# Kernel tuning notes

Measured on AMD Instinct MI355X. Metric: run time of the kernel, lower is better.

The kernel has to match this reference:

```python
import jax, jax.numpy as jnp
import numpy as np

B, T, C, H, D = 4, 2048, 1024, 16, 64  # batch, seq, n_embd, n_head, head_size


def setup_inputs() -> dict:
    key = jax.random.key(0)
    ks = jax.random.split(key, 8)
    s = 0.02  # init scale for weights
    return {
        "q": jax.random.normal(ks[0], (B, T, C), jnp.float32),
        "k": jax.random.normal(ks[1], (B, T, C), jnp.float32),
        "v": jax.random.normal(ks[2], (B, T, C), jnp.float32),
        "Wq": jax.random.normal(ks[3], (H, C, D), jnp.float32) * s,
        "Wk": jax.random.normal(ks[4], (H, C, D), jnp.float32) * s,
        "Wv": jax.random.normal(ks[5], (H, C, D), jnp.float32) * s,
        "Wo": jax.random.normal(ks[6], (H * D, C), jnp.float32) * s,
        "bo": jnp.zeros((C,), jnp.float32),
    }


def reference(q, k, v, Wq, Wk, Wv, Wo, bo):
    # Per-head projections (vectorized over heads): [B,T,C] x [H,C,D] -> [B,H,T,D]
    qh = jnp.einsum('btc,hcd->bhtd', q, Wq)
    kh = jnp.einsum('btc,hcd->bhtd', k, Wk)
    vh = jnp.einsum('btc,hcd->bhtd', v, Wv)
    # NOTE: source divides by sqrt(C) = sqrt(n_embd), not sqrt(head_size)
    scale = 1.0 / jnp.sqrt(jnp.float32(C))
    att = jnp.einsum('bhtd,bhsd->bhts', qh, kh) * scale  # [B,H,T,T]
    causal = jnp.tril(jnp.ones((T, T), dtype=bool))
    att = jnp.where(causal, att, -jnp.inf)
    p = jax.nn.softmax(att, axis=-1)  # dropout is identity in eval mode
    out = jnp.einsum('bhts,bhsd->bhtd', p, vh)
    # concat heads in order: [B,H,T,D] -> [B,T,H*D]
    out = out.transpose(0, 2, 1, 3).reshape(B, T, H * D)
    return out @ Wo + bo
```

## Files before the change

kernel.cpp:

```cpp
#include <hip/hip_runtime.h>
#include <hip/hip_bf16.h>
#include <cstdint>
#include <cstddef>

#define B_  4
#define T_  2048
#define C_  1024
#define H_  16
#define D_  64
#define MROWS (B_*T_)
#define NDIM  (H_*D_)

typedef float  f32x4 __attribute__((ext_vector_type(4)));
typedef __bf16 bfrag __attribute__((ext_vector_type(8)));

__device__ __forceinline__ unsigned short f2bf(float f) {
  union { float f; unsigned u; } v; v.f = f;
  unsigned r = v.u + 0x7fffu + ((v.u >> 16) & 1u);
  return (unsigned short)(r >> 16);
}

__device__ __forceinline__ void async_load16(const void* g, void* l) {
  __builtin_amdgcn_global_load_lds((__attribute__((address_space(1))) void*)(void*)g,
                                   (__attribute__((address_space(3))) void*)l,
                                   16, 0, 0);
}

__device__ __forceinline__ unsigned cvt_pk_bf16(float f0, float f1) {
  unsigned r;
  asm("v_cvt_pk_bf16_f32 %0, %1, %2" : "=v"(r) : "v"(f0), "v"(f1));
  return r;
}

__global__ __launch_bounds__(256) void prep_kernel(
    const float* __restrict__ q, const float* __restrict__ k, const float* __restrict__ v,
    unsigned short* __restrict__ qb, unsigned short* __restrict__ kb, unsigned short* __restrict__ vb,
    const float* __restrict__ Wq, const float* __restrict__ Wk, const float* __restrict__ Wv,
    unsigned short* __restrict__ wqT, unsigned short* __restrict__ wkT, unsigned short* __restrict__ wvT,
    const float* __restrict__ Wo, unsigned short* __restrict__ woT)
{
  const int id = blockIdx.x, tid = threadIdx.x;
  if (id < 3072) {
    int z = id >> 10, blk = id & 1023;
    const float* in = z == 0 ? q : z == 1 ? k : v;
    unsigned short* out = z == 0 ? qb : z == 1 ? kb : vb;
    int base = blk * 2048;
#pragma unroll
    for (int r2 = 0; r2 < 8; ++r2) {
      int i = (base + r2 * 256 + tid) * 4;
      float4 vv = *(const float4*)(in + i);
      ushort4 rr;
      rr.x = f2bf(vv.x); rr.y = f2bf(vv.y); rr.z = f2bf(vv.z); rr.w = f2bf(vv.w);
      *(ushort4*)(out + i) = rr;
    }
  } else if (id < 3840) {
    int u = id - 3072;
    int z = u >> 4, cblk = u & 15;
    int sel = z >> 4, h = z & 15;
    const float* in = (sel == 0 ? Wq : sel == 1 ? Wk : Wv) + (size_t)h * C_ * D_;
    unsigned short* out = (sel == 0 ? wqT : sel == 1 ? wkT : wvT) + (size_t)h * D_ * C_;
    __shared__ float tile[64][65];
    int c0 = cblk * 64;
    int x = tid & 63, y4 = tid >> 6;
    for (int r = y4; r < 64; r += 4)
      tile[r][x] = in[(size_t)(c0 + r) * D_ + x];
    __syncthreads();
    for (int r = y4; r < 64; r += 4)
      out[(size_t)r * C_ + c0 + x] = f2bf(tile[x][r]);
  } else {
    int u = id - 3840;
    __shared__ float tile[64][65];
    int i0 = (u >> 4) * 64, j0 = (u & 15) * 64;
    int x = tid & 63, y4 = tid >> 6;
    for (int r = y4; r < 64; r += 4)
      tile[r][x] = Wo[(size_t)(i0 + r) * C_ + j0 + x];
    __syncthreads();
    for (int r = y4; r < 64; r += 4)
      woT[(size_t)(j0 + r) * NDIM + i0 + x] = f2bf(tile[x][r]);
  }
}

__global__ __launch_bounds__(512, 4) void gemm_qkv(
    const unsigned short* __restrict__ A0, const unsigned short* __restrict__ A1, const unsigned short* __restrict__ A2,
    const unsigned short* __restrict__ B0, const unsigned short* __restrict__ B1, const unsigned short* __restrict__ B2,
    void* C0, void* C1, void* C2)
{
  constexpr int K = C_;
  constexpr int N = NDIM;
  __shared__ __align__(16) short As[256 * 64];
  __shared__ __align__(16) short Bs[128 * 64];

  const int id = blockIdx.x;
  const int xcd = id & 7, s = id >> 3;
  const int z = s >> 5;
  const int t = s & 31;
  const int mb = xcd * 4 + (t >> 3);
  const int nb = t & 7;

  const unsigned short* A  = z == 0 ? A0 : z == 1 ? A1 : A2;
  const unsigned short* Bt = z == 0 ? B0 : z == 1 ? B1 : B2;
  void* Cv                 = z == 0 ? C0 : z == 1 ? C1 : C2;

  const int tid = threadIdx.x, lane = tid & 63, wave = tid >> 6;
  const int quad = lane >> 4, l15 = lane & 15;
  const int m0 = mb * 256, n0 = nb * 128;
  const int wm = (wave >> 1) * 64, wn = (wave & 1) * 64;
  const int wbase = tid & ~63;

  f32x4 acc[4][4] = {};

  for (int k0 = 0; k0 < K; k0 += 64) {
#pragma unroll
    for (int i = 0; i < 4; ++i) {
      int p0 = i * 512 + wbase;
      int p = p0 + lane;
      int m = p >> 3, cl = (p & 7) ^ (m & 7);
      async_load16(A + (size_t)(m0 + m) * K + k0 + cl * 8, (char*)As + p0 * 16);
    }
#pragma unroll
    for (int i = 0; i < 2; ++i) {
      int p0 = i * 512 + wbase;
      int p = p0 + lane;
      int m = p >> 3, cl = (p & 7) ^ (m & 7);
      async_load16(Bt + (size_t)(n0 + m) * K + k0 + cl * 8, (char*)Bs + p0 * 16);
    }
    __syncthreads();
#pragma unroll
    for (int ks = 0; ks < 2; ++ks) {
      bfrag af[4], bf[4];
#pragma unroll
      for (int i = 0; i < 4; ++i) {
        int m = wm + i * 16 + l15;
        int c = (ks * 4 + quad) ^ (m & 7);
        af[i] = *(const bfrag*)(As + m * 64 + c * 8);
        int n = wn + i * 16 + l15;
        int c2 = (ks * 4 + quad) ^ (n & 7);
        bf[i] = *(const bfrag*)(Bs + n * 64 + c2 * 8);
      }
#pragma unroll
      for (int i = 0; i < 4; ++i)
#pragma unroll
        for (int j = 0; j < 4; ++j)
          acc[i][j] = __builtin_amdgcn_mfma_f32_16x16x32_bf16(af[i], bf[j], acc[i][j], 0, 0, 0);
    }
    __syncthreads();
  }

  if (z < 2) {
    const float sc = (z == 0) ? 0.045084220f : 1.0f;
    unsigned short* Cb = (unsigned short*)Cv;
#pragma unroll
    for (int i = 0; i < 4; ++i) {
      int row0 = m0 + wm + i * 16 + quad * 4;
#pragma unroll
      for (int j = 0; j < 4; ++j) {
        int col = n0 + wn + j * 16 + l15;
#pragma unroll
        for (int r = 0; r < 4; ++r)
          Cb[(size_t)(row0 + r) * N + col] = f2bf(acc[i][j][r] * sc);
      }
    }
  } else {
    unsigned short* Vo = (unsigned short*)Cv;
#pragma unroll
    for (int i = 0; i < 4; ++i) {
      int m = m0 + wm + i * 16 + quad * 4;
      int bb = m >> 11, tt = m & 2047;
#pragma unroll
      for (int j = 0; j < 4; ++j) {
        int n = n0 + wn + j * 16 + l15;
        int hh = n >> 6, dd = n & 63;
        ushort4 pk;
        pk.x = f2bf(acc[i][j][0]); pk.y = f2bf(acc[i][j][1]);
        pk.z = f2bf(acc[i][j][2]); pk.w = f2bf(acc[i][j][3]);
        *(ushort4*)(Vo + (((size_t)bb * 16 + hh) * 64 + dd) * T_ + tt) = pk;
      }
    }
  }
}

__global__ __launch_bounds__(256) void gemm_o(
    const unsigned short* __restrict__ A, const unsigned short* __restrict__ Bt,
    float* __restrict__ Cf, const float* __restrict__ bias)
{
  constexpr int K = NDIM;
  constexpr int N = C_;
  __shared__ __align__(16) short As[128 * 64];
  __shared__ __align__(16) short Bs[128 * 64];

  const int id = blockIdx.x;
  const int xcd = id & 7, t = id >> 3;
  const int mb = xcd * 8 + (t >> 3);
  const int nb = t & 7;

  const int tid = threadIdx.x, lane = tid & 63, wave = tid >> 6;
  const int quad = lane >> 4, l15 = lane & 15;
  const int m0 = mb * 128, n0 = nb * 128;
  const int wm = (wave >> 1) * 64, wn = (wave & 1) * 64;

  f32x4 acc[4][4] = {};

  for (int k0 = 0; k0 < K; k0 += 64) {
#pragma unroll
    for (int i = 0; i < 4; ++i) {
      int p0 = (wave * 4 + i) * 64;
      int p = p0 + lane;
      int m = p >> 3, cl = (p & 7) ^ (m & 7);
      async_load16(A  + (size_t)(m0 + m) * K + k0 + cl * 8, (char*)As + p0 * 16);
      async_load16(Bt + (size_t)(n0 + m) * K + k0 + cl * 8, (char*)Bs + p0 * 16);
    }
    __syncthreads();
#pragma unroll
    for (int ks = 0; ks < 2; ++ks) {
      bfrag af[4], bf[4];
#pragma unroll
      for (int i = 0; i < 4; ++i) {
        int m = wm + i * 16 + l15;
        int c = (ks * 4 + quad) ^ (m & 7);
        af[i] = *(const bfrag*)(As + m * 64 + c * 8);
        int n = wn + i * 16 + l15;
        int c2 = (ks * 4 + quad) ^ (n & 7);
        bf[i] = *(const bfrag*)(Bs + n * 64 + c2 * 8);
      }
#pragma unroll
      for (int i = 0; i < 4; ++i)
#pragma unroll
        for (int j = 0; j < 4; ++j)
          acc[i][j] = __builtin_amdgcn_mfma_f32_16x16x32_bf16(af[i], bf[j], acc[i][j], 0, 0, 0);
    }
    __syncthreads();
  }

#pragma unroll
  for (int j = 0; j < 4; ++j) {
    int col = n0 + wn + j * 16 + l15;
    float bv = bias[col];
#pragma unroll
    for (int i = 0; i < 4; ++i) {
      int row0 = m0 + wm + i * 16 + quad * 4;
#pragma unroll
      for (int r = 0; r < 4; ++r)
        Cf[(size_t)(row0 + r) * N + col] = acc[i][j][r] + bv;
    }
  }
}

__global__ __launch_bounds__(256, 3) void flash_kernel(
    const unsigned short* __restrict__ Qh, const unsigned short* __restrict__ Kh,
    const unsigned short* __restrict__ VT, unsigned short* __restrict__ Oh)
{
  __shared__ __align__(16) short Ks[128 * 64];
  __shared__ __align__(16) short Vt[2][64 * 64];
  __shared__ __align__(16) short Ps[4][32 * 64];

  const int tid = threadIdx.x, lane = tid & 63, wave = tid >> 6;
  const int quad = lane >> 4, l15 = lane & 15;
  const int id = blockIdx.x;
  const int rr = id >> 8, cc = id & 255, g = cc >> 6, bh = cc & 63;
  const int t = (rr == 0) ? g : (rr == 1) ? 7 - g : (rr == 2) ? 8 + g : 15 - g;
  const int b = bh >> 4, h = bh & 15;
  const int q0 = t * 128;

  const unsigned short* Qbase = Qh + (size_t)b * T_ * NDIM + h * 64;
  const unsigned short* Kbase = Kh + (size_t)b * T_ * NDIM + h * 64;
  const unsigned short* Vbase = VT + ((size_t)(b * 16 + h) * 64) * T_;

  const int wrow_lo = q0 + wave * 32;

  bfrag qfr[2][2];
#pragma unroll
  for (int j = 0; j < 2; ++j)
#pragma unroll
    for (int ks = 0; ks < 2; ++ks)
      qfr[j][ks] = *(const bfrag*)(Qbase + (size_t)(wrow_lo + j * 16 + l15) * NDIM + ks * 32 + quad * 8);

  float l_st[2] = {0.f, 0.f};
  f32x4 o_acc[2][4] = {};
  short* pw = &Ps[wave][0];

  for (int kv0 = 0; kv0 < q0 + 128; kv0 += 128) {
#pragma unroll
    for (int i = 0; i < 4; ++i) {
      int p0 = (wave * 4 + i) * 64;
      int p = p0 + lane;
      int kr = p >> 3, kcl = (p & 7) ^ (kr & 7);
      async_load16(Kbase + (size_t)(kv0 + kr) * NDIM + kcl * 8, (char*)Ks + p0 * 16);
      int hh = p >> 9, d = (p >> 3) & 63, vcl = (p & 7) ^ (d & 7);
      async_load16(Vbase + (size_t)d * T_ + kv0 + hh * 64 + vcl * 8, (char*)Vt + p0 * 16);
    }
    __syncthreads();

#pragma unroll
    for (int hf = 0; hf < 2; ++hf) {
      const int kvh = kv0 + hf * 64;
      if (kvh > wrow_lo + 31) break;

      f32x4 sv[2][4] = {};
#pragma unroll
      for (int ks = 0; ks < 2; ++ks) {
        bfrag kf[4];
#pragma unroll
        for (int i = 0; i < 4; ++i) {
          int key = i * 16 + l15;
          int c = (ks * 4 + quad) ^ (key & 7);
          kf[i] = *(const bfrag*)(Ks + (hf * 64 + key) * 64 + c * 8);
        }
#pragma unroll
        for (int j = 0; j < 2; ++j)
#pragma unroll
          for (int i = 0; i < 4; ++i)
            sv[j][i] = __builtin_amdgcn_mfma_f32_16x16x32_bf16(kf[i], qfr[j][ks], sv[j][i], 0, 0, 0);
      }

#pragma unroll
      for (int j = 0; j < 2; ++j)
#pragma unroll
        for (int i = 0; i < 4; ++i)
#pragma unroll
          for (int r = 0; r < 4; ++r)
            sv[j][i][r] = __builtin_amdgcn_exp2f(sv[j][i][r]);
      if (kvh + 63 > wrow_lo) {
#pragma unroll
        for (int j = 0; j < 2; ++j) {
          int qr = wrow_lo + j * 16 + l15;
#pragma unroll
          for (int i = 0; i < 4; ++i) {
            int keyb = kvh + i * 16 + quad * 4;
#pragma unroll
            for (int r = 0; r < 4; ++r)
              if (keyb + r > qr) sv[j][i][r] = 0.f;
          }
        }
      }

#pragma unroll
      for (int j = 0; j < 2; ++j) {
        int rowb = j * 16 + l15;
        short* prow = pw + rowb * 64;
        int rx = rowb & 7;
#pragma unroll
        for (int i = 0; i < 4; ++i) {
          l_st[j] += sv[j][i][0] + sv[j][i][1] + sv[j][i][2] + sv[j][i][3];
          uint2 pk;
          pk.x = cvt_pk_bf16(sv[j][i][0], sv[j][i][1]);
          pk.y = cvt_pk_bf16(sv[j][i][2], sv[j][i][3]);
          int cch = (i * 2 + (quad >> 1)) ^ rx;
          *(uint2*)(prow + cch * 8 + (quad & 1) * 4) = pk;
        }
      }

#pragma unroll
      for (int ks = 0; ks < 2; ++ks) {
        bfrag vf[4], pf[2];
#pragma unroll
        for (int i2 = 0; i2 < 4; ++i2) {
          int d = i2 * 16 + l15;
          int c = (ks * 4 + quad) ^ (d & 7);
          vf[i2] = *(const bfrag*)(&Vt[hf][0] + d * 64 + c * 8);
        }
#pragma unroll
        for (int j = 0; j < 2; ++j) {
          int rowb = j * 16 + l15;
          pf[j] = *(const bfrag*)(pw + rowb * 64 + (((ks * 4 + quad) ^ (rowb & 7)) * 8));
        }
#pragma unroll
        for (int j = 0; j < 2; ++j)
#pragma unroll
          for (int i2 = 0; i2 < 4; ++i2)
            o_acc[j][i2] = __builtin_amdgcn_mfma_f32_16x16x32_bf16(vf[i2], pf[j], o_acc[j][i2], 0, 0, 0);
      }
    }
    __syncthreads();
  }

#pragma unroll
  for (int j = 0; j < 2; ++j) {
    float s = l_st[j];
    s += __shfl_xor(s, 16, 64);
    s += __shfl_xor(s, 32, 64);
    float inv = 1.f / s;
    int qr = q0 + wave * 32 + j * 16 + l15;
    size_t base = ((size_t)b * T_ + qr) * NDIM + h * 64;
#pragma unroll
    for (int i2 = 0; i2 < 4; ++i2) {
      uint2 pk;
      pk.x = cvt_pk_bf16(o_acc[j][i2][0] * inv, o_acc[j][i2][1] * inv);
      pk.y = cvt_pk_bf16(o_acc[j][i2][2] * inv, o_acc[j][i2][3] * inv);
      *(uint2*)(Oh + base + i2 * 16 + quad * 4) = pk;
    }
  }
}

extern "C" void kernel_launch(void* const* d_in, const int* in_sizes, int n_in,
                              void* d_out, int out_size, void* d_ws, size_t ws_size,
                              hipStream_t stream)
{
  const float* q  = (const float*)d_in[0];
  const float* k  = (const float*)d_in[1];
  const float* v  = (const float*)d_in[2];
  const float* Wq = (const float*)d_in[3];
  const float* Wk = (const float*)d_in[4];
  const float* Wv = (const float*)d_in[5];
  const float* Wo = (const float*)d_in[6];
  const float* bo = (const float*)d_in[7];
  float* out = (float*)d_out;

  char* w = (char*)d_ws;
  const size_t szBTC = (size_t)MROWS * C_ * 2;
  const size_t szW   = (size_t)NDIM * C_ * 2;
  unsigned short* qb   = (unsigned short*)(w);
  unsigned short* kb   = (unsigned short*)(w + szBTC);
  unsigned short* vb   = (unsigned short*)(w + 2 * szBTC);
  unsigned short* wqT  = (unsigned short*)(w + 3 * szBTC);
  unsigned short* wkT  = (unsigned short*)(w + 3 * szBTC + szW);
  unsigned short* wvT  = (unsigned short*)(w + 3 * szBTC + 2 * szW);
  unsigned short* woT  = (unsigned short*)(w + 3 * szBTC + 3 * szW);
  unsigned short* qhp  = (unsigned short*)(w + 3 * szBTC + 4 * szW);
  unsigned short* khp  = (unsigned short*)(w + 4 * szBTC + 4 * szW);
  unsigned short* vT   = (unsigned short*)(w + 5 * szBTC + 4 * szW);
  unsigned short* attO = (unsigned short*)(w + 6 * szBTC + 4 * szW);

  prep_kernel<<<dim3(4096), 256, 0, stream>>>(q, k, v, qb, kb, vb,
                                              Wq, Wk, Wv, wqT, wkT, wvT, Wo, woT);

  gemm_qkv<<<dim3(768), 512, 0, stream>>>(
      qb, kb, vb, wqT, wkT, wvT, qhp, khp, vT);

  flash_kernel<<<dim3(1024), 256, 0, stream>>>(qhp, khp, vT, attO);

  gemm_o<<<dim3(512), 256, 0, stream>>>(attO, woT, out, bo);
}
```

Baseline: 295.4 us.

## Fuse fp32-to-bf16 activation conversion into QKV GEMM tile loads

Drops the separate pass that converted q/k/v from fp32 to bf16 in global memory. The QKV GEMM now async-loads fp32 tiles straight into LDS with a 16-way XOR swizzle and converts them to bf16 in registers before the MFMA. This removes a full write and re-read of three bf16 activation tensors. In exchange the GEMM moves twice the A-operand bytes per tile, needs double the A LDS footprint (64KB plus 16KB for B), which may cut occupancy, and adds conversion instructions to the inner loop.

```diff
diff --git a/kernel.cpp b/kernel.cpp
--- a/kernel.cpp
+++ b/kernel.cpp
@@ -33,28 +33,13 @@
 }
 
 __global__ __launch_bounds__(256) void prep_kernel(
-    const float* __restrict__ q, const float* __restrict__ k, const float* __restrict__ v,
-    unsigned short* __restrict__ qb, unsigned short* __restrict__ kb, unsigned short* __restrict__ vb,
     const float* __restrict__ Wq, const float* __restrict__ Wk, const float* __restrict__ Wv,
     unsigned short* __restrict__ wqT, unsigned short* __restrict__ wkT, unsigned short* __restrict__ wvT,
     const float* __restrict__ Wo, unsigned short* __restrict__ woT)
 {
   const int id = blockIdx.x, tid = threadIdx.x;
-  if (id < 3072) {
-    int z = id >> 10, blk = id & 1023;
-    const float* in = z == 0 ? q : z == 1 ? k : v;
-    unsigned short* out = z == 0 ? qb : z == 1 ? kb : vb;
-    int base = blk * 2048;
-#pragma unroll
-    for (int r2 = 0; r2 < 8; ++r2) {
-      int i = (base + r2 * 256 + tid) * 4;
-      float4 vv = *(const float4*)(in + i);
-      ushort4 rr;
-      rr.x = f2bf(vv.x); rr.y = f2bf(vv.y); rr.z = f2bf(vv.z); rr.w = f2bf(vv.w);
-      *(ushort4*)(out + i) = rr;
-    }
-  } else if (id < 3840) {
-    int u = id - 3072;
+  if (id < 768) {
+    int u = id;
     int z = u >> 4, cblk = u & 15;
     int sel = z >> 4, h = z & 15;
     const float* in = (sel == 0 ? Wq : sel == 1 ? Wk : Wv) + (size_t)h * C_ * D_;
@@ -68,7 +53,7 @@
     for (int r = y4; r < 64; r += 4)
       out[(size_t)r * C_ + c0 + x] = f2bf(tile[x][r]);
   } else {
-    int u = id - 3840;
+    int u = id - 768;
     __shared__ float tile[64][65];
     int i0 = (u >> 4) * 64, j0 = (u & 15) * 64;
     int x = tid & 63, y4 = tid >> 6;
@@ -81,13 +66,13 @@
 }
 
 __global__ __launch_bounds__(512, 4) void gemm_qkv(
-    const unsigned short* __restrict__ A0, const unsigned short* __restrict__ A1, const unsigned short* __restrict__ A2,
+    const float* __restrict__ A0, const float* __restrict__ A1, const float* __restrict__ A2,
     const unsigned short* __restrict__ B0, const unsigned short* __restrict__ B1, const unsigned short* __restrict__ B2,
     void* C0, void* C1, void* C2)
 {
   constexpr int K = C_;
   constexpr int N = NDIM;
-  __shared__ __align__(16) short As[256 * 64];
+  __shared__ __align__(16) float As[256 * 64];
   __shared__ __align__(16) short Bs[128 * 64];
 
   const int id = blockIdx.x;
@@ -97,7 +82,7 @@
   const int mb = xcd * 4 + (t >> 3);
   const int nb = t & 7;
 
-  const unsigned short* A  = z == 0 ? A0 : z == 1 ? A1 : A2;
+  const float* A           = z == 0 ? A0 : z == 1 ? A1 : A2;
   const unsigned short* Bt = z == 0 ? B0 : z == 1 ? B1 : B2;
   void* Cv                 = z == 0 ? C0 : z == 1 ? C1 : C2;
 
@@ -111,11 +96,11 @@
 
   for (int k0 = 0; k0 < K; k0 += 64) {
 #pragma unroll
-    for (int i = 0; i < 4; ++i) {
+    for (int i = 0; i < 8; ++i) {
       int p0 = i * 512 + wbase;
       int p = p0 + lane;
-      int m = p >> 3, cl = (p & 7) ^ (m & 7);
-      async_load16(A + (size_t)(m0 + m) * K + k0 + cl * 8, (char*)As + p0 * 16);
+      int m = p >> 4, cl = (p & 15) ^ (m & 15);
+      async_load16(A + (size_t)(m0 + m) * K + k0 + cl * 4, (char*)As + p0 * 16);
     }
 #pragma unroll
     for (int i = 0; i < 2; ++i) {
@@ -131,8 +116,16 @@
 #pragma unroll
       for (int i = 0; i < 4; ++i) {
         int m = wm + i * 16 + l15;
-        int c = (ks * 4 + quad) ^ (m & 7);
-        af[i] = *(const bfrag*)(As + m * 64 + c * 8);
+        int j0c = (ks * 4 + quad) * 2;
+        const float* pA = As + m * 64;
+        f32x4 a0 = *(const f32x4*)(pA + ((j0c ^ (m & 15)) << 2));
+        f32x4 a1 = *(const f32x4*)(pA + (((j0c + 1) ^ (m & 15)) << 2));
+        union { unsigned u[4]; bfrag b; } cv;
+        cv.u[0] = cvt_pk_bf16(a0[0], a0[1]);
+        cv.u[1] = cvt_pk_bf16(a0[2], a0[3]);
+        cv.u[2] = cvt_pk_bf16(a1[0], a1[1]);
+        cv.u[3] = cvt_pk_bf16(a1[2], a1[3]);
+        af[i] = cv.b;
         int n = wn + i * 16 + l15;
         int c2 = (ks * 4 + quad) ^ (n & 7);
         bf[i] = *(const bfrag*)(Bs + n * 64 + c2 * 8);
@@ -408,9 +401,6 @@
   char* w = (char*)d_ws;
   const size_t szBTC = (size_t)MROWS * C_ * 2;
   const size_t szW   = (size_t)NDIM * C_ * 2;
-  unsigned short* qb   = (unsigned short*)(w);
-  unsigned short* kb   = (unsigned short*)(w + szBTC);
-  unsigned short* vb   = (unsigned short*)(w + 2 * szBTC);
   unsigned short* wqT  = (unsigned short*)(w + 3 * szBTC);
   unsigned short* wkT  = (unsigned short*)(w + 3 * szBTC + szW);
   unsigned short* wvT  = (unsigned short*)(w + 3 * szBTC + 2 * szW);
@@ -420,11 +410,10 @@
   unsigned short* vT   = (unsigned short*)(w + 5 * szBTC + 4 * szW);
   unsigned short* attO = (unsigned short*)(w + 6 * szBTC + 4 * szW);
 
-  prep_kernel<<<dim3(4096), 256, 0, stream>>>(q, k, v, qb, kb, vb,
-                                              Wq, Wk, Wv, wqT, wkT, wvT, Wo, woT);
+  prep_kernel<<<dim3(1024), 256, 0, stream>>>(Wq, Wk, Wv, wqT, wkT, wvT, Wo, woT);
 
   gemm_qkv<<<dim3(768), 512, 0, stream>>>(
-      qb, kb, vb, wqT, wkT, wvT, qhp, khp, vT);
+      q, k, v, wqT, wkT, wvT, qhp, khp, vT);
 
   flash_kernel<<<dim3(1024), 256, 0, stream>>>(qhp, khp, vT, attO);
 
```

Result: slower. 310.5 us (+5.1%).
